# Kernel tuning notes

Measured on AMD Instinct MI355X. Metric: run time of the kernel, lower is better.

The kernel has to match this reference:

```python
import jax, jax.numpy as jnp
import numpy as np

D_MODEL = 1024
D_STATE = 16
D_CONV = 4
EXPAND = 2
D_INNER = D_MODEL * EXPAND          # 2048
DT_RANK = max(1, D_MODEL // 16)     # 64
BATCH, SEQ = 4, 2048


def setup_inputs() -> dict:
    key = jax.random.key(0)
    ks = jax.random.split(key, 8)
    s = lambda n: 1.0 / np.sqrt(n)
    x = jax.random.normal(ks[0], (BATCH, SEQ, D_MODEL), jnp.float32)
    in_proj_w = jax.random.normal(ks[1], (2 * D_INNER, D_MODEL), jnp.float32) * s(D_MODEL)
    conv_w = jax.random.normal(ks[2], (D_INNER, 1, D_CONV), jnp.float32) * s(D_CONV)
    conv_b = jax.random.normal(ks[3], (D_INNER,), jnp.float32) * 0.01
    x_proj_w = jax.random.normal(ks[4], (DT_RANK + 2 * D_STATE, D_INNER), jnp.float32) * s(D_INNER)
    dt_proj_w = jax.random.normal(ks[5], (D_INNER, DT_RANK), jnp.float32) * s(DT_RANK)
    dt_proj_b = jax.random.normal(ks[6], (D_INNER,), jnp.float32) * 0.01
    A_log = jnp.broadcast_to(jnp.log(jnp.arange(1, D_STATE + 1, dtype=jnp.float32))[None, :],
                             (D_INNER, D_STATE)).copy()
    D_param = jnp.ones((D_INNER,), jnp.float32)
    out_proj_w = jax.random.normal(ks[7], (D_MODEL, D_INNER), jnp.float32) * s(D_INNER)
    return {"x": x, "in_proj_w": in_proj_w, "conv_w": conv_w, "conv_b": conv_b,
            "x_proj_w": x_proj_w, "dt_proj_w": dt_proj_w, "dt_proj_b": dt_proj_b,
            "A_log": A_log, "D_param": D_param, "out_proj_w": out_proj_w}


def _ssm_forward(x, in_proj_w, conv_w, conv_b, x_proj_w, dt_proj_w, dt_proj_b,
                 A_log, D_param, out_proj_w):
    B, L, _ = x.shape
    # input projection -> (B, L, 2*D_INNER), split into x_ssm and gate z
    xz = jnp.einsum('bld,ed->ble', x, in_proj_w)
    x_ssm, z = xz[..., :D_INNER], xz[..., D_INNER:]
    # causal depthwise conv1d (torch pads both sides then slices [:L] == left pad only)
    xc = jnp.transpose(x_ssm, (0, 2, 1))  # (B, D_INNER, L)
    xc = jax.lax.conv_general_dilated(
        xc, conv_w, window_strides=(1,), padding=[(D_CONV - 1, 0)],
        dimension_numbers=('NCH', 'OIH', 'NCH'), feature_group_count=D_INNER)
    xc = xc + conv_b[None, :, None]
    x_ssm = jax.nn.silu(jnp.transpose(xc, (0, 2, 1)))  # (B, L, D_INNER)
    # input-dependent dt, B, C
    dbl = jnp.einsum('bld,ed->ble', x_ssm, x_proj_w)  # (B, L, DT_RANK+2N)
    dt_x = dbl[..., :DT_RANK]
    B_x = dbl[..., DT_RANK:DT_RANK + D_STATE]
    C_x = dbl[..., DT_RANK + D_STATE:]
    dt = jax.nn.softplus(jnp.einsum('blr,dr->bld', dt_x, dt_proj_w) + dt_proj_b)  # (B, L, D_INNER)
    A = -jnp.exp(A_log)  # (D_INNER, D_STATE)

    # selective scan over L with lax.scan; carry h: (B, D_INNER, D_STATE)
    def step(h, inp):
        dt_t, B_t, C_t, x_t = inp  # (B,D), (B,N), (B,N), (B,D)
        dA = jnp.exp(dt_t[:, :, None] * A[None, :, :])          # (B, D, N)
        dB = dt_t[:, :, None] * B_t[:, None, :]                 # (B, D, N)
        h = dA * h + dB * x_t[:, :, None]
        y_t = jnp.einsum('bdn,bn->bd', h, C_t)
        return h, y_t

    h0 = jnp.zeros((B, D_INNER, D_STATE), x.dtype)
    xs = (jnp.moveaxis(dt, 1, 0), jnp.moveaxis(B_x, 1, 0),
          jnp.moveaxis(C_x, 1, 0), jnp.moveaxis(x_ssm, 1, 0))
    _, ys = jax.lax.scan(step, h0, xs)          # ys: (L, B, D_INNER)
    y = jnp.moveaxis(ys, 0, 1) + D_param[None, None, :] * x_ssm
    y = y * jax.nn.silu(z)
    return jnp.einsum('ble,de->bld', y, out_proj_w)


def reference(x, in_proj_w, conv_w, conv_b, x_proj_w, dt_proj_w, dt_proj_b,
              A_log, D_param, out_proj_w):
    return _ssm_forward(x, in_proj_w, conv_w, conv_b, x_proj_w, dt_proj_w,
                        dt_proj_b, A_log, D_param, out_proj_w)
```

## Files before the change

### kernel.cpp

```cpp
#include <hip/hip_runtime.h>
#include <hip/hip_bf16.h>
#include <math.h>

#define D_MODEL 1024
#define D_STATE 16
#define D_CONV 4
#define D_INNER 2048
#define DT_RANK 64
#define BATCH 4
#define SEQ 2048
#define ML (BATCH * SEQ)
#define NCH 64
#define CL (SEQ / NCH)

typedef __attribute__((ext_vector_type(8))) short short8;
typedef __attribute__((ext_vector_type(8))) unsigned short u16x8;
typedef __attribute__((ext_vector_type(4))) float f32x4;

__device__ __forceinline__ float bf2f(unsigned short u) {
  union { unsigned int i; float f; } v;
  v.i = ((unsigned int)u) << 16;
  return v.f;
}
__device__ __forceinline__ unsigned short f2bf(float f) {
  union { float f; unsigned int i; } u;
  u.f = f;
  unsigned int r = u.i + 0x7fffu + ((u.i >> 16) & 1u);
  return (unsigned short)(r >> 16);
}
__device__ __forceinline__ unsigned int f2bf_pk(float a, float b) {
  union { __hip_bfloat162 h; unsigned int u; } cv;
  cv.h = __float22bfloat162_rn(make_float2(a, b));
  return cv.u;
}
template <bool BF>
__device__ __forceinline__ float ld1(const void* p, size_t i) {
  if constexpr (BF) return bf2f(((const unsigned short*)p)[i]);
  else return ((const float*)p)[i];
}
template <bool BF>
__device__ __forceinline__ void ld4(const void* p, size_t i, float o[4]) {
  if constexpr (BF) {
    ushort4 v = *(const ushort4*)((const unsigned short*)p + i);
    o[0] = bf2f(v.x); o[1] = bf2f(v.y); o[2] = bf2f(v.z); o[3] = bf2f(v.w);
  } else {
    float4 v = *(const float4*)((const float*)p + i);
    o[0] = v.x; o[1] = v.y; o[2] = v.z; o[3] = v.w;
  }
}

__device__ __forceinline__ void gl_lds16(const unsigned short* g,
                                         unsigned short* l) {
  __builtin_amdgcn_global_load_lds(
      (const __attribute__((address_space(1))) void*)g,
      (__attribute__((address_space(3))) void*)l, 16, 0, 0);
}

__global__ void detect_kernel(const unsigned int* __restrict__ xw, int* flag) {
  __shared__ int cnt;
  if (threadIdx.x == 0) cnt = 0;
  __syncthreads();
  unsigned int w = xw[threadIdx.x];
  unsigned int e = (w >> 7) & 0xffu;
  if (e < 100u || e > 145u) atomicAdd(&cnt, 1);
  __syncthreads();
  if (threadIdx.x == 0) flag[0] = (cnt < 32) ? 1 : 0;
}

#define CVT_N0 (ML * 1024)
#define CVT_N1 (4096 * 1024)
#define CVT_N2 (1024 * 2048)
#define CVT_N3 (2048 * 64)
#define CVT_N4 (128 * 2048)
#define CVT_E0 CVT_N0
#define CVT_E1 (CVT_E0 + CVT_N1)
#define CVT_E2 (CVT_E1 + CVT_N2)
#define CVT_E3 (CVT_E2 + CVT_N3)
#define CVT_E4 (CVT_E3 + CVT_N4)

__device__ __forceinline__ void cvt4(const void* in, size_t i,
                                     unsigned short* out, size_t o, int bf) {
  if (bf) {
    *(ushort4*)(out + o) = *(const ushort4*)((const unsigned short*)in + i);
  } else {
    float4 f = *(const float4*)((const float*)in + i);
    uint2 v;
    v.x = f2bf_pk(f.x, f.y);
    v.y = f2bf_pk(f.z, f.w);
    *(uint2*)(out + o) = v;
  }
}

__global__ __launch_bounds__(256) void cvt_all_kernel(
    const void* __restrict__ x, const void* __restrict__ ipw,
    const void* __restrict__ opw, const void* __restrict__ dtw,
    const void* __restrict__ xpw, unsigned short* __restrict__ x_bf,
    unsigned short* __restrict__ ipw_bf, unsigned short* __restrict__ opw_bf,
    unsigned short* __restrict__ dtw_bf, unsigned short* __restrict__ xpw_pad,
    const int* __restrict__ flag) {
  const int bf = *flag;
  const size_t g = (size_t)(blockIdx.x * 256 + threadIdx.x) * 4;
  if (g < CVT_E0) {
    cvt4(x, g, x_bf, g, bf);
  } else if (g < CVT_E1) {
    const size_t i = g - CVT_E0;
    cvt4(ipw, i, ipw_bf, i, bf);
  } else if (g < CVT_E2) {
    const size_t i = g - CVT_E1;
    cvt4(opw, i, opw_bf, i, bf);
  } else if (g < CVT_E3) {
    const size_t i = g - CVT_E2;
    cvt4(dtw, i, dtw_bf, i, bf);
  } else if (g < CVT_E4) {
    const size_t i = g - CVT_E3;
    const int row = (int)(i >> 11);
    if (row < 96) {
      cvt4(xpw, i, xpw_pad, i, bf);
    } else {
      ushort4 z = {0, 0, 0, 0};
      *(ushort4*)(xpw_pad + i) = z;
    }
  }
}

#define K1_LDA 1024
#define K1_NT 16

#define K1_STG(srcbase, lds, t_, h_)                                       \
  {                                                                        \
    const unsigned short* s_ =                                             \
        (srcbase) + (size_t)(h_) * (128 * K1_LDA) + (size_t)(t_) * 64;     \
    unsigned short* d_ = (lds) + (((t_) & 1) * 2 + (h_)) * 8192 + w * 512; \
    gl_lds16(s_, d_);                                                      \
    gl_lds16(s_ + 64 * K1_LDA, d_ + 4096);                                 \
  }

__global__ __launch_bounds__(512, 2) void gemm256_k1(
    const unsigned short* __restrict__ A,
    const unsigned short* __restrict__ B,
    unsigned short* __restrict__ C) {
  __shared__ unsigned short As[32768];
  __shared__ unsigned short Bs[32768];
  const int tid = threadIdx.x;
  const int l = tid & 63, w = tid >> 6;
  const int bid = blockIdx.x;
  const int swz = (bid & 7) * 64 + (bid >> 3);
  const int m0 = (swz >> 4) * 256, n0 = (swz & 15) * 256;
  const int row0 = tid >> 3;
  const int c0 = (tid & 7) ^ (row0 & 7);
  const unsigned short* aSrc = A + (size_t)(m0 + row0) * K1_LDA + c0 * 8;
  const unsigned short* bSrc = B + (size_t)(n0 + row0) * K1_LDA + c0 * 8;
  const int q = l >> 4, mr = l & 15;
  const int wm = w >> 2, wn = w & 3;

  K1_STG(aSrc, As, 0, 0);
  K1_STG(aSrc, As, 0, 1);
  K1_STG(bSrc, Bs, 0, 0);
  K1_STG(bSrc, Bs, 0, 1);
  K1_STG(bSrc, Bs, 1, 0);
  K1_STG(bSrc, Bs, 1, 1);
  K1_STG(aSrc, As, 1, 0);
  asm volatile("s_waitcnt vmcnt(6)" ::: "memory");
  asm volatile("s_barrier" ::: "memory");

  f32x4 acc[8][4] = {};
  for (int t = 0; t < K1_NT; ++t) {
    const int tb = (t & 1) * 2;
    short8 bfr[4][2];
#pragma unroll
    for (int ni = 0; ni < 4; ++ni)
#pragma unroll
      for (int kk = 0; kk < 2; ++kk) {
        const int r = (wn & 1) * 64 + ni * 16 + mr;
        const int c = kk * 4 + q;
        bfr[ni][kk] = *(const short8*)&Bs[(tb + (wn >> 1)) * 8192 + r * 64 +
                                          ((c ^ (r & 7)) * 8)];
      }
#pragma unroll
    for (int p = 0; p < 4; ++p) {
      short8 af[2][2];
#pragma unroll
      for (int i = 0; i < 2; ++i)
#pragma unroll
        for (int kk = 0; kk < 2; ++kk) {
          const int r = (2 * p + i) * 16 + mr;
          const int c = kk * 4 + q;
          af[i][kk] = *(const short8*)&As[(tb + wm) * 8192 + r * 64 +
                                          ((c ^ (r & 7)) * 8)];
        }
      if (p == 0) {
        if (t + 1 < K1_NT) K1_STG(aSrc, As, t + 1, 1);
      } else if (p == 1) {
        if (t + 2 < K1_NT) K1_STG(bSrc, Bs, t + 2, 0);
      } else if (p == 2) {
        if (t + 2 < K1_NT) K1_STG(bSrc, Bs, t + 2, 1);
      } else {
        if (t + 2 < K1_NT) K1_STG(aSrc, As, t + 2, 0);
      }
      asm volatile("s_barrier" ::: "memory");
      __builtin_amdgcn_s_setprio(1);
#pragma unroll
      for (int i = 0; i < 2; ++i)
#pragma unroll
        for (int ni = 0; ni < 4; ++ni)
#pragma unroll
          for (int kk = 0; kk < 2; ++kk)
            acc[2 * p + i][ni] = __builtin_amdgcn_mfma_f32_16x16x32_bf16(
                af[i][kk], bfr[ni][kk], acc[2 * p + i][ni], 0, 0, 0);
      __builtin_amdgcn_s_setprio(0);
      if (p == 3) {
        if (t + 2 < K1_NT) {
          asm volatile("s_waitcnt vmcnt(6)" ::: "memory");
        } else {
          asm volatile("s_waitcnt vmcnt(0)" ::: "memory");
        }
      }
      asm volatile("s_barrier" ::: "memory");
    }
  }
#pragma unroll
  for (int mi = 0; mi < 8; ++mi) {
#pragma unroll
    for (int ni = 0; ni < 4; ++ni) {
      const int row = m0 + wm * 128 + mi * 16 + q * 4;
      const int col = n0 + wn * 64 + ni * 16 + mr;
      const size_t off0 = (size_t)row * 4096 + col;
      const unsigned int p01 = f2bf_pk(acc[mi][ni][0], acc[mi][ni][1]);
      const unsigned int p23 = f2bf_pk(acc[mi][ni][2], acc[mi][ni][3]);
      C[off0] = (unsigned short)p01;
      C[off0 + 4096] = (unsigned short)(p01 >> 16);
      C[off0 + 2 * 4096] = (unsigned short)p23;
      C[off0 + 3 * 4096] = (unsigned short)(p23 >> 16);
    }
  }
}

#define K6_LDA 2048
#define K6_NT 32

#define K6_STGA(t_, h_)                                                 \
  {                                                                     \
    const unsigned short* s_ =                                          \
        aSrc + (size_t)(h_) * (128 * K6_LDA) + (size_t)(t_) * 64;       \
    unsigned short* d_ = As + (((t_) & 1) * 2 + (h_)) * 8192 + w * 512; \
    gl_lds16(s_, d_);                                                   \
    gl_lds16(s_ + 64 * K6_LDA, d_ + 4096);                              \
  }
#define K6_STGB(t_)                                            \
  {                                                            \
    const unsigned short* s_ = bSrc + (size_t)(t_) * 64;       \
    unsigned short* d_ = Bs6 + ((t_) & 1) * 8192 + w * 512;    \
    gl_lds16(s_, d_);                                          \
    gl_lds16(s_ + 64 * K6_LDA, d_ + 4096);                     \
  }

__global__ __launch_bounds__(512, 2) void gemm256x128_k6(
    const unsigned short* __restrict__ A,
    const unsigned short* __restrict__ B,
    void* __restrict__ C,
    const int* __restrict__ flag) {
  __shared__ unsigned short As[32768];
  __shared__ unsigned short Bs6[16384];
  const int tid = threadIdx.x;
  const int l = tid & 63, w = tid >> 6;
  const int bid = blockIdx.x;
  const int swz = (bid & 7) * 32 + (bid >> 3);
  const int n0 = (swz & 7) * 128, m0 = (swz >> 3) * 256;
  const int row0 = tid >> 3;
  const int c0 = (tid & 7) ^ (row0 & 7);
  const unsigned short* aSrc = A + (size_t)(m0 + row0) * K6_LDA + c0 * 8;
  const unsigned short* bSrc = B + (size_t)(n0 + row0) * K6_LDA + c0 * 8;
  const int q = l >> 4, mr = l & 15;
  const int wm = w >> 2, wn = w & 3;

  K6_STGA(0, 0);
  K6_STGA(0, 1);
  K6_STGB(0);
  K6_STGB(1);
  K6_STGA(1, 0);
  asm volatile("s_waitcnt vmcnt(4)" ::: "memory");
  asm volatile("s_barrier" ::: "memory");

  f32x4 acc[8][2] = {};
  for (int t = 0; t < K6_NT; ++t) {
    const int tb = (t & 1) * 2;
    short8 bfr[2][2];
#pragma unroll
    for (int ni = 0; ni < 2; ++ni)
#pragma unroll
      for (int kk = 0; kk < 2; ++kk) {
        const int r = wn * 32 + ni * 16 + mr;
        const int c = kk * 4 + q;
        bfr[ni][kk] = *(const short8*)&Bs6[(t & 1) * 8192 + r * 64 +
                                           ((c ^ (r & 7)) * 8)];
      }
#pragma unroll
    for (int p = 0; p < 4; ++p) {
      short8 af[2][2];
#pragma unroll
      for (int i = 0; i < 2; ++i)
#pragma unroll
        for (int kk = 0; kk < 2; ++kk) {
          const int r = (2 * p + i) * 16 + mr;
          const int c = kk * 4 + q;
          af[i][kk] = *(const short8*)&As[(tb + wm) * 8192 + r * 64 +
                                          ((c ^ (r & 7)) * 8)];
        }
      if (p == 0) {
        if (t + 1 < K6_NT) K6_STGA(t + 1, 1);
      } else if (p == 1) {
        if (t + 2 < K6_NT) K6_STGB(t + 2);
      } else if (p == 3) {
        if (t + 2 < K6_NT) K6_STGA(t + 2, 0);
      }
      asm volatile("s_barrier" ::: "memory");
      __builtin_amdgcn_s_setprio(1);
#pragma unroll
      for (int i = 0; i < 2; ++i)
#pragma unroll
        for (int ni = 0; ni < 2; ++ni)
#pragma unroll
          for (int kk = 0; kk < 2; ++kk)
            acc[2 * p + i][ni] = __builtin_amdgcn_mfma_f32_16x16x32_bf16(
                af[i][kk], bfr[ni][kk], acc[2 * p + i][ni], 0, 0, 0);
      __builtin_amdgcn_s_setprio(0);
      if (p == 3) {
        if (t + 2 < K6_NT) {
          asm volatile("s_waitcnt vmcnt(4)" ::: "memory");
        } else {
          asm volatile("s_waitcnt vmcnt(0)" ::: "memory");
        }
      }
      asm volatile("s_barrier" ::: "memory");
    }
  }
  const int bf = *flag;
#pragma unroll
  for (int mi = 0; mi < 8; ++mi) {
#pragma unroll
    for (int ni = 0; ni < 2; ++ni) {
      const int row = m0 + wm * 128 + mi * 16 + q * 4;
      const int col = n0 + wn * 32 + ni * 16 + mr;
      const size_t off0 = (size_t)row * 1024 + col;
      if (bf) {
        const unsigned int p01 = f2bf_pk(acc[mi][ni][0], acc[mi][ni][1]);
        const unsigned int p23 = f2bf_pk(acc[mi][ni][2], acc[mi][ni][3]);
        unsigned short* C16 = (unsigned short*)C;
        C16[off0] = (unsigned short)p01;
        C16[off0 + 1024] = (unsigned short)(p01 >> 16);
        C16[off0 + 2 * 1024] = (unsigned short)p23;
        C16[off0 + 3 * 1024] = (unsigned short)(p23 >> 16);
      } else {
        float* Cf = (float*)C;
#pragma unroll
        for (int j = 0; j < 4; ++j)
          Cf[off0 + (size_t)j * 1024] = acc[mi][ni][j];
      }
    }
  }
}

__global__ __launch_bounds__(256) void dt_gemm_kernel(
    const unsigned short* __restrict__ Adbl,
    const unsigned short* __restrict__ Bw,
    unsigned short* __restrict__ Cdt,
    const void* __restrict__ bias, const int* __restrict__ flag) {
  __shared__ unsigned short Bs[128 * 64];
  __shared__ unsigned short Ass[4][128 * 64];
  const int tid = threadIdx.x;
  const int l = tid & 63, w = tid >> 6;
  const int bn = blockIdx.x * 128;
  const int mg = blockIdx.y * 512;
  const int srow = tid >> 3;
  const int sc = ((tid & 7) ^ (srow & 7)) * 8;
  const unsigned short* aSrc = Adbl + (size_t)(mg + srow) * 128 + sc;
  const unsigned short* bSrc = Bw + (size_t)(bn + srow) * 64 + sc;
#define K4_STGB(i_) gl_lds16(bSrc + (i_) * 32 * 64, Bs + (i_)*2048 + w * 512)
#define K4_STGA(mt_, i_)                                  \
  gl_lds16(aSrc + (size_t)((mt_)*128 + (i_)*32) * 128,    \
           Ass[(mt_) & 3] + (i_)*2048 + w * 512)
  K4_STGB(0); K4_STGB(1); K4_STGB(2); K4_STGB(3);
  K4_STGA(0, 0); K4_STGA(0, 1); K4_STGA(0, 2); K4_STGA(0, 3);
  K4_STGA(1, 0); K4_STGA(1, 1); K4_STGA(1, 2); K4_STGA(1, 3);
  asm volatile("s_waitcnt vmcnt(4)" ::: "memory");
  asm volatile("s_barrier" ::: "memory");
  const int q = l >> 4, mr = l & 15;
  const int wm = w >> 1, wn = w & 1;
  short8 bfr[4][2];
#pragma unroll
  for (int ni = 0; ni < 4; ++ni)
#pragma unroll
    for (int kk = 0; kk < 2; ++kk) {
      const int r = wn * 64 + ni * 16 + mr;
      const int c = kk * 4 + q;
      bfr[ni][kk] = *(const short8*)&Bs[r * 64 + ((c ^ (r & 7)) * 8)];
    }
  const int bf = *flag;
  float bv[4];
#pragma unroll
  for (int ni = 0; ni < 4; ++ni) {
    const int col = bn + wn * 64 + ni * 16 + mr;
    bv[ni] = bf ? ld1<true>(bias, col) : ld1<false>(bias, col);
  }
#pragma unroll
  for (int mt = 0; mt < 4; ++mt) {
    if (mt + 2 < 4) {
      K4_STGA(mt + 2, 0); K4_STGA(mt + 2, 1);
      K4_STGA(mt + 2, 2); K4_STGA(mt + 2, 3);
    }
    short8 af[4][2];
#pragma unroll
    for (int mi = 0; mi < 4; ++mi)
#pragma unroll
      for (int kk = 0; kk < 2; ++kk) {
        const int r = wm * 64 + mi * 16 + mr;
        const int c = kk * 4 + q;
        af[mi][kk] =
            *(const short8*)&Ass[mt & 3][r * 64 + ((c ^ (r & 7)) * 8)];
      }
    f32x4 acc[4][4] = {};
#pragma unroll
    for (int mi = 0; mi < 4; ++mi)
#pragma unroll
      for (int ni = 0; ni < 4; ++ni)
#pragma unroll
        for (int kk = 0; kk < 2; ++kk)
          acc[mi][ni] = __builtin_amdgcn_mfma_f32_16x16x32_bf16(
              af[mi][kk], bfr[ni][kk], acc[mi][ni], 0, 0, 0);
#pragma unroll
    for (int mi = 0; mi < 4; ++mi) {
#pragma unroll
      for (int ni = 0; ni < 4; ++ni) {
        const int row = mg + mt * 128 + wm * 64 + mi * 16 + q * 4;
        const int col = bn + wn * 64 + ni * 16 + mr;
        const size_t off0 = (size_t)row * 4096 + col;
        float v[4];
#pragma unroll
        for (int j = 0; j < 4; ++j) {
          const float t = acc[mi][ni][j] + bv[ni];
          v[j] = fmaxf(t, 0.f) + __logf(1.f + __expf(-fabsf(t)));
        }
        const unsigned int p01 = f2bf_pk(v[0], v[1]);
        const unsigned int p23 = f2bf_pk(v[2], v[3]);
        Cdt[off0] = (unsigned short)p01;
        Cdt[off0 + 4096] = (unsigned short)(p01 >> 16);
        Cdt[off0 + 2 * 4096] = (unsigned short)p23;
        Cdt[off0 + 3 * 4096] = (unsigned short)(p23 >> 16);
      }
    }
    if (mt + 2 < 4) {
      asm volatile("s_waitcnt vmcnt(4)" ::: "memory");
    } else {
      asm volatile("s_waitcnt vmcnt(0)" ::: "memory");
    }
    if (mt < 3) asm volatile("s_barrier" ::: "memory");
  }
}

template <int EPI, int TAG>
__global__ __launch_bounds__(256) void gemm_mfma(
    const unsigned short* __restrict__ Ain, int lda,
    const unsigned short* __restrict__ Bin, int ldb, void* __restrict__ C,
    int ldc, int K, const void* __restrict__ bias,
    const int* __restrict__ flag) {
  __shared__ unsigned short As[128 * 32];
  __shared__ unsigned short Bs[128 * 32];
  const unsigned short* A = Ain;
  const unsigned short* B = Bin;
  if (EPI == 3) {
    A += (size_t)blockIdx.z * 512;
    B += (size_t)blockIdx.z * 512;
  }
  const int tid = threadIdx.x;
  const int l = tid & 63, w = tid >> 6;
  const int bm = blockIdx.y * 128;
  const int bn = blockIdx.x * 128;
  const int r0 = w * 16 + (l >> 2);
  const int cc = (((l & 3) ^ ((l >> 2) & 3) ^ ((l >> 4) & 3))) * 8;
  const unsigned short* Ap0 = A + (size_t)(bm + r0) * lda + cc;
  const unsigned short* Ap1 = A + (size_t)(bm + r0 + 64) * lda + cc;
  const unsigned short* Bp0 = B + (size_t)(bn + r0) * ldb + cc;
  const unsigned short* Bp1 = B + (size_t)(bn + r0 + 64) * ldb + cc;
  const int q = l >> 4, mr = l & 15;
  const int wm = w >> 1, wn = w & 1;
  const int slot = (q ^ (mr & 3) ^ (mr >> 2)) * 8;
  f32x4 acc[4][4] = {};
  for (int k0 = 0; k0 < K; k0 += 32) {
    gl_lds16(Ap0 + k0, As + w * 512);
    gl_lds16(Ap1 + k0, As + 2048 + w * 512);
    gl_lds16(Bp0 + k0, Bs + w * 512);
    gl_lds16(Bp1 + k0, Bs + 2048 + w * 512);
    __syncthreads();
    short8 af[4], bfr[4];
#pragma unroll
    for (int mi = 0; mi < 4; ++mi)
      af[mi] = *(const short8*)&As[(wm * 64 + mi * 16 + mr) * 32 + slot];
#pragma unroll
    for (int ni = 0; ni < 4; ++ni)
      bfr[ni] = *(const short8*)&Bs[(wn * 64 + ni * 16 + mr) * 32 + slot];
#pragma unroll
    for (int mi = 0; mi < 4; ++mi)
#pragma unroll
      for (int ni = 0; ni < 4; ++ni)
        acc[mi][ni] = __builtin_amdgcn_mfma_f32_16x16x32_bf16(
            af[mi], bfr[ni], acc[mi][ni], 0, 0, 0);
    __syncthreads();
  }
  const int bf = (EPI == 1) ? *flag : 0;
  float* Cp3 = (EPI == 3)
                   ? ((float*)C + (size_t)blockIdx.z * ML * 128)
                   : (float*)C;
#pragma unroll
  for (int mi = 0; mi < 4; ++mi) {
#pragma unroll
    for (int ni = 0; ni < 4; ++ni) {
      const int row = bm + wm * 64 + mi * 16 + q * 4;
      const int col = bn + wn * 64 + ni * 16 + mr;
      const size_t off0 = (size_t)row * ldc + col;
      if (EPI == 0) {
        const unsigned int p01 = f2bf_pk(acc[mi][ni][0], acc[mi][ni][1]);
        const unsigned int p23 = f2bf_pk(acc[mi][ni][2], acc[mi][ni][3]);
        unsigned short* C16 = (unsigned short*)C;
        C16[off0] = (unsigned short)p01;
        C16[off0 + ldc] = (unsigned short)(p01 >> 16);
        C16[off0 + 2 * (size_t)ldc] = (unsigned short)p23;
        C16[off0 + 3 * (size_t)ldc] = (unsigned short)(p23 >> 16);
      } else if (EPI == 3) {
#pragma unroll
        for (int j = 0; j < 4; ++j)
          Cp3[off0 + (size_t)j * ldc] = acc[mi][ni][j];
      } else {
        if (bf) {
          const unsigned int p01 = f2bf_pk(acc[mi][ni][0], acc[mi][ni][1]);
          const unsigned int p23 = f2bf_pk(acc[mi][ni][2], acc[mi][ni][3]);
          unsigned short* C16 = (unsigned short*)C;
          C16[off0] = (unsigned short)p01;
          C16[off0 + ldc] = (unsigned short)(p01 >> 16);
          C16[off0 + 2 * (size_t)ldc] = (unsigned short)p23;
          C16[off0 + 3 * (size_t)ldc] = (unsigned short)(p23 >> 16);
        } else {
          float* Cf = (float*)C;
#pragma unroll
          for (int j = 0; j < 4; ++j)
            Cf[off0 + (size_t)j * ldc] = acc[mi][ni][j];
        }
      }
    }
  }
}

__global__ __launch_bounds__(256) void reduceK3_kernel(
    const float* __restrict__ part, unsigned short* __restrict__ dbl) {
  const size_t i = (size_t)(blockIdx.x * 256 + threadIdx.x) * 4;
  const size_t st = (size_t)ML * 128;
  float4 a = *(const float4*)(part + i);
  float4 b = *(const float4*)(part + st + i);
  float4 c = *(const float4*)(part + 2 * st + i);
  float4 d = *(const float4*)(part + 3 * st + i);
  uint2 v;
  v.x = f2bf_pk(a.x + b.x + c.x + d.x, a.y + b.y + c.y + d.y);
  v.y = f2bf_pk(a.z + b.z + c.z + d.z, a.w + b.w + c.w + d.w);
  *(uint2*)(dbl + i) = v;
}

__global__ __launch_bounds__(256) void conv_silu_kernel(
    const unsigned short* __restrict__ xzb, const void* __restrict__ cw,
    const void* __restrict__ cb, unsigned short* __restrict__ xcb,
    const int* __restrict__ flag) {
  const int bf = *flag;
  const int e = (blockIdx.x * 256 + threadIdx.x) * 4;
  const int d = e & (D_INNER - 1);
  const int bl = e >> 11;
  const int l = bl & (SEQ - 1);
  const size_t base = (size_t)bl * 4096 + d;
  float x0[4], x1[4] = {}, x2[4] = {}, x3[4] = {};
  ld4<true>(xzb, base, x0);
  if (l >= 1) ld4<true>(xzb, base - 4096, x1);
  if (l >= 2) ld4<true>(xzb, base - 2 * 4096, x2);
  if (l >= 3) ld4<true>(xzb, base - 3 * 4096, x3);
  float r[4];
#pragma unroll
  for (int i = 0; i < 4; ++i) {
    float w[4];
    if (bf) ld4<true>(cw, (size_t)(d + i) * 4, w);
    else ld4<false>(cw, (size_t)(d + i) * 4, w);
    const float bias = bf ? ld1<true>(cb, d + i) : ld1<false>(cb, d + i);
    float acc = bias + w[3] * x0[i] + w[2] * x1[i] + w[1] * x2[i] + w[0] * x3[i];
    r[i] = acc / (1.f + __expf(-acc));
  }
  uint2 o;
  o.x = f2bf_pk(r[0], r[1]);
  o.y = f2bf_pk(r[2], r[3]);
  *(uint2*)(xcb + e) = o;
}

__device__ __forceinline__ void load_a(const void* A_log, int bf, int d,
                                       float a[16], float& dev) {
  float t[4];
#pragma unroll
  for (int k = 0; k < 4; ++k) {
    if (bf) ld4<true>(A_log, (size_t)d * 16 + k * 4, t);
    else ld4<false>(A_log, (size_t)d * 16 + k * 4, t);
#pragma unroll
    for (int j = 0; j < 4; ++j) a[k * 4 + j] = -expf(t[j]);
  }
  dev = 0.f;
#pragma unroll
  for (int n = 0; n < 16; ++n) dev = fmaxf(dev, fabsf(a[n] + (float)(n + 1)));
}

__device__ __forceinline__ void pow_tree(float e1, float pw[16]) {
  const float e2 = e1 * e1;
  const float e3 = e2 * e1;
  const float e4 = e2 * e2;
  pw[0] = e1; pw[1] = e2; pw[2] = e3; pw[3] = e4;
  pw[4] = e4 * e1; pw[5] = e4 * e2; pw[6] = e4 * e3; pw[7] = e4 * e4;
  const float e8 = pw[7];
  pw[8] = e8 * e1; pw[9] = e8 * e2; pw[10] = e8 * e3; pw[11] = e8 * e4;
  pw[12] = e8 * pw[4]; pw[13] = e8 * pw[5]; pw[14] = e8 * pw[6];
  pw[15] = e8 * e8;
}

__global__ __launch_bounds__(256) void scan_passA(
    const unsigned short* __restrict__ xzb,
    const unsigned short* __restrict__ xcb,
    const unsigned short* __restrict__ dbl, const void* __restrict__ A_log,
    const int* __restrict__ flag, float* __restrict__ S,
    float* __restrict__ P) {
  const int bf = *flag;
  const int gid = blockIdx.x * 256 + threadIdx.x;
  const int d = gid & (D_INNER - 1);
  const int c = (gid >> 11) & (NCH - 1);
  const int b = gid >> 17;
  float a[16], dev;
  load_a(A_log, bf, d, a, dev);
  float h[16] = {};
  float sdt = 0.f;
  const size_t m0 = (size_t)b * SEQ + c * CL;
  if (dev < 1e-3f) {
    for (int t = 0; t < CL; ++t) {
      const size_t m = m0 + t;
      const float dtv = bf2f(xzb[m * 4096 + d]);
      const float xv = bf2f(xcb[m * 2048 + d]);
      const u16x8 B0 = *(const u16x8*)&dbl[m * 128 + 64];
      const u16x8 B1 = *(const u16x8*)&dbl[m * 128 + 72];
      const float dtx = dtv * xv;
      sdt += dtv;
      float pw[16];
      pow_tree(__expf(-dtv), pw);
#pragma unroll
      for (int n = 0; n < 16; ++n) {
        const float Bv = bf2f(n < 8 ? B0[n] : B1[n - 8]);
        h[n] = fmaf(pw[n], h[n], Bv * dtx);
      }
    }
  } else {
    for (int t = 0; t < CL; ++t) {
      const size_t m = m0 + t;
      const float dtv = bf2f(xzb[m * 4096 + d]);
      const float xv = bf2f(xcb[m * 2048 + d]);
      const u16x8 B0 = *(const u16x8*)&dbl[m * 128 + 64];
      const u16x8 B1 = *(const u16x8*)&dbl[m * 128 + 72];
      const float dtx = dtv * xv;
      sdt += dtv;
#pragma unroll
      for (int n = 0; n < 16; ++n) {
        const float Bv = bf2f(n < 8 ? B0[n] : B1[n - 8]);
        h[n] = fmaf(__expf(dtv * a[n]), h[n], Bv * dtx);
      }
    }
  }
  const size_t sidx = (((size_t)b * NCH + c) * D_INNER + d) * 16;
#pragma unroll
  for (int n = 0; n < 16; ++n) {
    S[sidx + n] = h[n];
    P[sidx + n] = __expf(a[n] * sdt);
  }
}

__global__ __launch_bounds__(256) void scan_passB(float* __restrict__ S,
                                                  const float* __restrict__ P) {
  const int idx = blockIdx.x * 256 + threadIdx.x;
  const int n = idx & 15;
  const int d = (idx >> 4) & (D_INNER - 1);
  const int b = idx >> 15;
  float h = 0.f;
  for (int c = 0; c < NCH; ++c) {
    const size_t sidx = (((size_t)b * NCH + c) * D_INNER + d) * 16 + n;
    const float s = S[sidx], p = P[sidx];
    S[sidx] = h;
    h = p * h + s;
  }
}

__global__ __launch_bounds__(256) void scan_passC(
    const unsigned short* __restrict__ xzb,
    const unsigned short* __restrict__ xcb,
    const unsigned short* __restrict__ dbl, const void* __restrict__ A_log,
    const void* __restrict__ Dp, const float* __restrict__ S,
    const int* __restrict__ flag, unsigned short* __restrict__ ybf) {
  const int bf = *flag;
  const int gid = blockIdx.x * 256 + threadIdx.x;
  const int d = gid & (D_INNER - 1);
  const int c = (gid >> 11) & (NCH - 1);
  const int b = gid >> 17;
  float a[16], dev;
  load_a(A_log, bf, d, a, dev);
  const float Dv = bf ? ld1<true>(Dp, d) : ld1<false>(Dp, d);
  float h[16];
  const size_t sidx = (((size_t)b * NCH + c) * D_INNER + d) * 16;
#pragma unroll
  for (int n = 0; n < 16; ++n) h[n] = S[sidx + n];
  const size_t m0 = (size_t)b * SEQ + c * CL;
  const bool trick = dev < 1e-3f;
  for (int t = 0; t < CL; ++t) {
    const size_t m = m0 + t;
    const float dtv = bf2f(xzb[m * 4096 + d]);
    const float xv = bf2f(xcb[m * 2048 + d]);
    const u16x8 B0 = *(const u16x8*)&dbl[m * 128 + 64];
    const u16x8 B1 = *(const u16x8*)&dbl[m * 128 + 72];
    const u16x8 C0 = *(const u16x8*)&dbl[m * 128 + 80];
    const u16x8 C1 = *(const u16x8*)&dbl[m * 128 + 88];
    const float dtx = dtv * xv;
    float y = 0.f;
    if (trick) {
      float pw[16];
      pow_tree(__expf(-dtv), pw);
#pragma unroll
      for (int n = 0; n < 16; ++n) {
        const float Bv = bf2f(n < 8 ? B0[n] : B1[n - 8]);
        const float Cv = bf2f(n < 8 ? C0[n] : C1[n - 8]);
        h[n] = fmaf(pw[n], h[n], Bv * dtx);
        y = fmaf(h[n], Cv, y);
      }
    } else {
#pragma unroll
      for (int n = 0; n < 16; ++n) {
        const float Bv = bf2f(n < 8 ? B0[n] : B1[n - 8]);
        const float Cv = bf2f(n < 8 ? C0[n] : C1[n - 8]);
        h[n] = fmaf(__expf(dtv * a[n]), h[n], Bv * dtx);
        y = fmaf(h[n], Cv, y);
      }
    }
    const float zv = bf2f(xzb[m * 4096 + 2048 + d]);
    const float yv = y + Dv * xv;
    ybf[m * 2048 + d] = f2bf(yv * (zv / (1.f + __expf(-zv))));
  }
}

extern "C" void kernel_launch(void* const* d_in, const int* in_sizes, int n_in,
                              void* d_out, int out_size, void* d_ws,
                              size_t ws_size, hipStream_t stream) {
  const void* x = d_in[0];
  const void* in_proj_w = d_in[1];
  const void* conv_w = d_in[2];
  const void* conv_b = d_in[3];
  const void* x_proj_w = d_in[4];
  const void* dt_proj_w = d_in[5];
  const void* dt_proj_b = d_in[6];
  const void* A_log = d_in[7];
  const void* D_param = d_in[8];
  const void* out_proj_w = d_in[9];

  char* wsb = (char*)d_ws;
  int* flag = (int*)wsb;
  unsigned short* xzb = (unsigned short*)(wsb + 256);
  unsigned short* xcb = xzb + (size_t)ML * 4096;
  unsigned short* dbl = xcb + (size_t)ML * 2048;
  unsigned short* ybf = dbl + (size_t)ML * 128;
  float* S = (float*)(ybf + (size_t)ML * 2048);
  float* P = S + (size_t)BATCH * NCH * D_INNER * 16;
  unsigned short* opw_bf =
      (unsigned short*)(P + (size_t)BATCH * NCH * D_INNER * 16);
  unsigned short* xpw_pad = opw_bf + (size_t)1024 * 2048;
  unsigned short* dtw_bf = xpw_pad + (size_t)128 * 2048;
  unsigned short* x_bf = xcb;
  unsigned short* ipw_bf = xcb + (size_t)ML * 1024;
  float* k3part = S;

  detect_kernel<<<1, 256, 0, stream>>>((const unsigned int*)x, flag);
  cvt_all_kernel<<<CVT_E4 / 1024, 256, 0, stream>>>(
      x, in_proj_w, out_proj_w, dt_proj_w, x_proj_w, x_bf, ipw_bf, opw_bf,
      dtw_bf, xpw_pad, flag);
  gemm256_k1<<<dim3(512), 512, 0, stream>>>(x_bf, ipw_bf, xzb);
  conv_silu_kernel<<<(ML * D_INNER) / 1024, 256, 0, stream>>>(
      xzb, conv_w, conv_b, xcb, flag);
  {
    dim3 g(1, ML / 128, 4);
    gemm_mfma<3, 3><<<g, 256, 0, stream>>>(xcb, 2048, xpw_pad, 2048, k3part,
                                           128, 512, nullptr, flag);
  }
  reduceK3_kernel<<<(ML * 128) / 1024, 256, 0, stream>>>(k3part, dbl);
  dt_gemm_kernel<<<dim3(16, 16), 256, 0, stream>>>(dbl, dtw_bf, xzb,
                                                   dt_proj_b, flag);
  scan_passA<<<(BATCH * NCH * D_INNER) / 256, 256, 0, stream>>>(
      xzb, xcb, dbl, A_log, flag, S, P);
  scan_passB<<<(BATCH * D_INNER * 16) / 256, 256, 0, stream>>>(S, P);
  scan_passC<<<(BATCH * NCH * D_INNER) / 256, 256, 0, stream>>>(
      xzb, xcb, dbl, A_log, D_param, S, flag, ybf);
  gemm256x128_k6<<<dim3(256), 512, 0, stream>>>(ybf, opw_bf, d_out, flag);
}
```

Baseline: 472.5 us.

## Fold dtype detection into convert kernel and shrink scan carry traffic

The separate dtype-detect kernel is removed. Every block of the convert kernel now recomputes the flag from the first 256 words of x, and block 0 writes it for later kernels. The scan chunk-state layout changes from d-major to n-major so that stores and loads across d are coalesced. Pass A stores only the per-chunk dt sum instead of 16 decay products, and pass B recomputes the decays with exp. This removes one launch and about half of the inter-pass state traffic, at the cost of redundant detection work in every convert block and extra exps in pass B.

```diff
diff --git a/kernel.cpp b/kernel.cpp
--- a/kernel.cpp
+++ b/kernel.cpp
@@ -56,17 +56,6 @@
       (__attribute__((address_space(3))) void*)l, 16, 0, 0);
 }
 
-__global__ void detect_kernel(const unsigned int* __restrict__ xw, int* flag) {
-  __shared__ int cnt;
-  if (threadIdx.x == 0) cnt = 0;
-  __syncthreads();
-  unsigned int w = xw[threadIdx.x];
-  unsigned int e = (w >> 7) & 0xffu;
-  if (e < 100u || e > 145u) atomicAdd(&cnt, 1);
-  __syncthreads();
-  if (threadIdx.x == 0) flag[0] = (cnt < 32) ? 1 : 0;
-}
-
 #define CVT_N0 (ML * 1024)
 #define CVT_N1 (4096 * 1024)
 #define CVT_N2 (1024 * 2048)
@@ -97,8 +86,19 @@
     const void* __restrict__ xpw, unsigned short* __restrict__ x_bf,
     unsigned short* __restrict__ ipw_bf, unsigned short* __restrict__ opw_bf,
     unsigned short* __restrict__ dtw_bf, unsigned short* __restrict__ xpw_pad,
-    const int* __restrict__ flag) {
-  const int bf = *flag;
+    int* __restrict__ flag) {
+  __shared__ int cnt;
+  if (threadIdx.x == 0) cnt = 0;
+  __syncthreads();
+  {
+    const unsigned int wv = ((const unsigned int*)x)[threadIdx.x];
+    const unsigned int e = (wv >> 7) & 0xffu;
+    if (e < 100u || e > 145u) atomicAdd(&cnt, 1);
+  }
+  __syncthreads();
+  const int bf = (cnt < 32) ? 1 : 0;
+  if (blockIdx.x == 0 && threadIdx.x == 0) flag[0] = bf;
+
   const size_t g = (size_t)(blockIdx.x * 256 + threadIdx.x) * 4;
   if (g < CVT_E0) {
     cvt4(x, g, x_bf, g, bf);
@@ -626,7 +626,7 @@
     const unsigned short* __restrict__ xcb,
     const unsigned short* __restrict__ dbl, const void* __restrict__ A_log,
     const int* __restrict__ flag, float* __restrict__ S,
-    float* __restrict__ P) {
+    float* __restrict__ Sdt) {
   const int bf = *flag;
   const int gid = blockIdx.x * 256 + threadIdx.x;
   const int d = gid & (D_INNER - 1);
@@ -670,24 +670,30 @@
       }
     }
   }
-  const size_t sidx = (((size_t)b * NCH + c) * D_INNER + d) * 16;
-#pragma unroll
-  for (int n = 0; n < 16; ++n) {
-    S[sidx + n] = h[n];
-    P[sidx + n] = __expf(a[n] * sdt);
-  }
-}
-
-__global__ __launch_bounds__(256) void scan_passB(float* __restrict__ S,
-                                                  const float* __restrict__ P) {
+  const size_t sbase = (((size_t)b * NCH + c) * 16) * D_INNER + d;
+#pragma unroll
+  for (int n = 0; n < 16; ++n) S[sbase + (size_t)n * D_INNER] = h[n];
+  Sdt[((size_t)b * NCH + c) * D_INNER + d] = sdt;
+}
+
+__global__ __launch_bounds__(256) void scan_passB(
+    float* __restrict__ S, const float* __restrict__ Sdt,
+    const void* __restrict__ A_log, const int* __restrict__ flag) {
+  const int bf = *flag;
   const int idx = blockIdx.x * 256 + threadIdx.x;
-  const int n = idx & 15;
-  const int d = (idx >> 4) & (D_INNER - 1);
+  const int d = idx & (D_INNER - 1);
+  const int n = (idx >> 11) & 15;
   const int b = idx >> 15;
+  const float al = bf ? ld1<true>(A_log, (size_t)d * 16 + n)
+                      : ld1<false>(A_log, (size_t)d * 16 + n);
+  const float a = -expf(al);
   float h = 0.f;
   for (int c = 0; c < NCH; ++c) {
-    const size_t sidx = (((size_t)b * NCH + c) * D_INNER + d) * 16 + n;
-    const float s = S[sidx], p = P[sidx];
+    const size_t base = ((size_t)b * NCH + c);
+    const size_t sidx = (base * 16 + n) * D_INNER + d;
+    const float s = S[sidx];
+    const float sdt = Sdt[base * D_INNER + d];
+    const float p = __expf(a * sdt);
     S[sidx] = h;
     h = p * h + s;
   }
@@ -708,9 +714,9 @@
   load_a(A_log, bf, d, a, dev);
   const float Dv = bf ? ld1<true>(Dp, d) : ld1<false>(Dp, d);
   float h[16];
-  const size_t sidx = (((size_t)b * NCH + c) * D_INNER + d) * 16;
-#pragma unroll
-  for (int n = 0; n < 16; ++n) h[n] = S[sidx + n];
+  const size_t sbase = (((size_t)b * NCH + c) * 16) * D_INNER + d;
+#pragma unroll
+  for (int n = 0; n < 16; ++n) h[n] = S[sbase + (size_t)n * D_INNER];
   const size_t m0 = (size_t)b * SEQ + c * CL;
   const bool trick = dev < 1e-3f;
   for (int t = 0; t < CL; ++t) {
@@ -769,16 +775,15 @@
   unsigned short* dbl = xcb + (size_t)ML * 2048;
   unsigned short* ybf = dbl + (size_t)ML * 128;
   float* S = (float*)(ybf + (size_t)ML * 2048);
-  float* P = S + (size_t)BATCH * NCH * D_INNER * 16;
+  float* Sdt = S + (size_t)BATCH * NCH * D_INNER * 16;
   unsigned short* opw_bf =
-      (unsigned short*)(P + (size_t)BATCH * NCH * D_INNER * 16);
+      (unsigned short*)(Sdt + (size_t)BATCH * NCH * D_INNER * 16);
   unsigned short* xpw_pad = opw_bf + (size_t)1024 * 2048;
   unsigned short* dtw_bf = xpw_pad + (size_t)128 * 2048;
   unsigned short* x_bf = xcb;
   unsigned short* ipw_bf = xcb + (size_t)ML * 1024;
   float* k3part = S;
 
-  detect_kernel<<<1, 256, 0, stream>>>((const unsigned int*)x, flag);
   cvt_all_kernel<<<CVT_E4 / 1024, 256, 0, stream>>>(
       x, in_proj_w, out_proj_w, dt_proj_w, x_proj_w, x_bf, ipw_bf, opw_bf,
       dtw_bf, xpw_pad, flag);
@@ -794,8 +799,9 @@
   dt_gemm_kernel<<<dim3(16, 16), 256, 0, stream>>>(dbl, dtw_bf, xzb,
                                                    dt_proj_b, flag);
   scan_passA<<<(BATCH * NCH * D_INNER) / 256, 256, 0, stream>>>(
-      xzb, xcb, dbl, A_log, flag, S, P);
-  scan_passB<<<(BATCH * D_INNER * 16) / 256, 256, 0, stream>>>(S, P);
+      xzb, xcb, dbl, A_log, flag, S, Sdt);
+  scan_passB<<<(BATCH * D_INNER * 16) / 256, 256, 0, stream>>>(S, Sdt, A_log,
+                                                               flag);
   scan_passC<<<(BATCH * NCH * D_INNER) / 256, 256, 0, stream>>>(
       xzb, xcb, dbl, A_log, D_param, S, flag, ybf);
   gemm256x128_k6<<<dim3(256), 512, 0, stream>>>(ybf, opw_bf, d_out, flag);
```

Measured after the change: 438.1 us. 7.3% less time.
